# Optimization experiments

Measured on AMD Instinct MI355X. Metric: run time of the kernel, lower is better.

The kernel has to match this reference:

```python
import jax, jax.numpy as jnp
import numpy as np
from jax import lax

B, T, V, D, H = 32, 128, 32000, 512, 512


def setup_inputs() -> dict:
    key = jax.random.key(0)
    ks = jax.random.split(key, 8)
    s = 0.05  # keep gate pre-activations in a sane range
    return {
        "dst": jax.random.randint(ks[0], (B, T), 0, V),
        "E": jax.random.normal(ks[1], (V, D), jnp.float32) * s,
        "W_ih": jax.random.normal(ks[2], (4 * H, D + H), jnp.float32) * s,
        "W_hh": jax.random.normal(ks[3], (4 * H, H), jnp.float32) * s,
        "b_ih": jnp.zeros((4 * H,), jnp.float32),
        "b_hh": jnp.zeros((4 * H,), jnp.float32),
        "h0": jax.random.normal(ks[4], (B, H), jnp.float32) * s,
        "c0": jax.random.normal(ks[5], (B, H), jnp.float32) * s,
        "out0": jax.random.normal(ks[6], (B, H), jnp.float32) * s,
    }


def reference(dst, E, W_ih, W_hh, b_ih, b_hh, h0, c0, out0):
    # Embed targets: [B, T, D] -> time-major [T, B, D]
    emb_tbd = jnp.swapaxes(E[dst], 0, 1)

    def step(carry, e_t):
        h, c, out_prev = carry
        # input feeding: concat embedding with previous output -> [B, D+H]
        x = jnp.concatenate([e_t, out_prev], axis=1)
        gates = x @ W_ih.T + b_ih + h @ W_hh.T + b_hh  # [B, 4H]
        i, f, g, o = jnp.split(gates, 4, axis=1)
        i = jax.nn.sigmoid(i)
        f = jax.nn.sigmoid(f)
        g = jnp.tanh(g)
        o = jax.nn.sigmoid(o)
        c_new = f * c + i * g
        h_new = o * jnp.tanh(c_new)
        # attn is identity; dropout disabled (p=0 / eval)
        return (h_new, c_new, h_new), h_new

    _, outs_tbh = lax.scan(step, (h0, c0, out0), emb_tbd)  # [T, B, H]
    out_bth = jnp.swapaxes(outs_tbh, 0, 1)  # [B, T, H]
    # weight-tied projection to vocab + log softmax
    logits = jnp.einsum("bth,vh->btv", out_bth, E)  # [B, T, V]
    return jax.nn.log_softmax(logits, axis=-1)
```

## Files before the change

kernel.cpp:

```cpp
#include <hip/hip_runtime.h>
#include <hip/hip_bf16.h>
#include <math.h>

#define B_ 32
#define T_ 128
#define V_ 32000
#define D_ 512
#define H_ 512

typedef __attribute__((ext_vector_type(8))) short bf16x8;
typedef __attribute__((ext_vector_type(4))) float f32x4;
typedef __attribute__((ext_vector_type(2))) unsigned long long u64x2;

#define AS1 __attribute__((address_space(1)))
#define AS3 __attribute__((address_space(3)))

__device__ __forceinline__ unsigned short f2bf(float x) {
  unsigned int b = __float_as_uint(x);
  return (unsigned short)((b + 0x7FFFu + ((b >> 16) & 1u)) >> 16);
}
__device__ __forceinline__ float bf2f(unsigned short u) {
  return __uint_as_float(((unsigned int)u) << 16);
}
__device__ __forceinline__ float sigm(float x) { return 1.0f / (1.0f + __expf(-x)); }
__device__ __forceinline__ float tanh_fast(float x) { return 1.0f - 2.0f / (__expf(2.0f * x) + 1.0f); }

__device__ __forceinline__ unsigned long long ald64(const unsigned long long* p) {
  return __hip_atomic_load(p, __ATOMIC_RELAXED, __HIP_MEMORY_SCOPE_AGENT);
}
__device__ __forceinline__ unsigned ald32(const unsigned* p) {
  return __hip_atomic_load(p, __ATOMIC_RELAXED, __HIP_MEMORY_SCOPE_AGENT);
}

__global__ __launch_bounds__(64) void embed_bf_kernel(const int* __restrict__ dst,
                                                      const float* __restrict__ E,
                                                      unsigned short* __restrict__ embbf) {
  int rt = blockIdx.x;
  int t = rt >> 5, b = rt & 31;
  int v = dst[b * T_ + t];
  const float4* src = (const float4*)(E + (size_t)v * D_);
  ushort4* d = (ushort4*)(embbf + (size_t)rt * D_);
  #pragma unroll
  for (int r = 0; r < 2; ++r) {
    float4 x = src[threadIdx.x + r * 64];
    ushort4 o; o.x = f2bf(x.x); o.y = f2bf(x.y); o.z = f2bf(x.z); o.w = f2bf(x.w);
    d[threadIdx.x + r * 64] = o;
  }
}

__global__ void cvt_kernel(const float* __restrict__ in, unsigned short* __restrict__ out, int n4) {
  int stride = gridDim.x * blockDim.x;
  for (int i = blockIdx.x * blockDim.x + threadIdx.x; i < n4; i += stride) {
    float4 v = ((const float4*)in)[i];
    ushort4 o; o.x = f2bf(v.x); o.y = f2bf(v.y); o.z = f2bf(v.z); o.w = f2bf(v.w);
    ((ushort4*)out)[i] = o;
  }
}

__global__ void cvt_w1_kernel(const float* __restrict__ Wih, unsigned short* __restrict__ W1bf, int n4) {
  int stride = gridDim.x * blockDim.x;
  for (int i = blockIdx.x * blockDim.x + threadIdx.x; i < n4; i += stride) {
    int flat = i * 4;
    int r = flat >> 9, c = flat & 511;
    float4 v = *(const float4*)(Wih + (size_t)r * 1024 + c);
    ushort4 o; o.x = f2bf(v.x); o.y = f2bf(v.y); o.z = f2bf(v.z); o.w = f2bf(v.w);
    ((ushort4*)W1bf)[i] = o;
  }
}

__global__ void wr_prep_swz_kernel(const float* __restrict__ Wih, const float* __restrict__ Whh,
                                   unsigned short* __restrict__ Wrs, int n4) {
  int stride = gridDim.x * blockDim.x;
  for (int i = blockIdx.x * blockDim.x + threadIdx.x; i < n4; i += stride) {
    int flat = i * 4;
    int grow = flat >> 9, k = flat & 511;
    float4 a = *(const float4*)(Wih + (size_t)grow * 1024 + 512 + k);
    float4 b = ((const float4*)Whh)[i];
    ushort4 o;
    o.x = f2bf(a.x + b.x); o.y = f2bf(a.y + b.y); o.z = f2bf(a.z + b.z); o.w = f2bf(a.w + b.w);
    int gate = grow >> 9, kgl = grow & 511;
    int orow = (kgl >> 5) * 128 + (kgl & 31) * 4 + gate;
    int chunk = (k >> 3) ^ (orow & 7);
    *(ushort4*)(Wrs + (size_t)orow * 512 + chunk * 8 + (k & 7)) = o;
  }
}

__global__ __launch_bounds__(256) void gemm_pre_kernel(
    const unsigned short* __restrict__ A,
    const unsigned short* __restrict__ Bm,
    const float* __restrict__ bih, const float* __restrict__ bhh,
    unsigned short* __restrict__ preA3)
{
  __shared__ unsigned short ldsA[2][128 * 32];
  __shared__ unsigned short ldsB[2][128 * 32];
  const int tid = threadIdx.x;
  const int lane = tid & 63;
  const int wid = tid >> 6;
  const int wm = wid >> 1, wn = wid & 1;
  const int m0 = blockIdx.y * 128;
  const int n0 = blockIdx.x * 128;
  const int srow = lane >> 2;
  const int scol = (lane & 3) * 8;

  f32x4 acc[4][4] = {};
  const int NK = 512 / 32;

  auto stage = [&](int kk, int buf) {
    const int k0 = kk * 32;
    #pragma unroll
    for (int c = 0; c < 2; ++c) {
      const int r = wid * 32 + c * 16;
      const unsigned short* sa = A  + (size_t)(m0 + r + srow) * 512 + k0 + scol;
      const unsigned short* sb = Bm + (size_t)(n0 + r + srow) * 512 + k0 + scol;
      __builtin_amdgcn_global_load_lds((const AS1 void*)sa, (AS3 void*)&ldsA[buf][r * 32], 16, 0, 0);
      __builtin_amdgcn_global_load_lds((const AS1 void*)sb, (AS3 void*)&ldsB[buf][r * 32], 16, 0, 0);
    }
  };

  stage(0, 0);
  __syncthreads();

  const int rl = lane & 15;
  const int kb = lane >> 4;

  for (int kk = 0; kk < NK; ++kk) {
    const int buf = kk & 1;
    if (kk + 1 < NK) stage(kk + 1, buf ^ 1);
    const bf16x8* Af = (const bf16x8*)&ldsA[buf][0];
    const bf16x8* Bf = (const bf16x8*)&ldsB[buf][0];
    bf16x8 av[4], bv[4];
    #pragma unroll
    for (int mi = 0; mi < 4; ++mi) av[mi] = Af[(wm * 64 + mi * 16 + rl) * 4 + kb];
    #pragma unroll
    for (int ni = 0; ni < 4; ++ni) bv[ni] = Bf[(wn * 64 + ni * 16 + rl) * 4 + kb];
    #pragma unroll
    for (int mi = 0; mi < 4; ++mi)
      #pragma unroll
      for (int ni = 0; ni < 4; ++ni)
        acc[mi][ni] = __builtin_amdgcn_mfma_f32_16x16x32_bf16(av[mi], bv[ni], acc[mi][ni], 0, 0, 0);
    __syncthreads();
  }

  const int rb = (lane >> 4) * 4;
  #pragma unroll
  for (int mi = 0; mi < 4; ++mi)
    #pragma unroll
    for (int ni = 0; ni < 4; ++ni) {
      int mbase = m0 + wm * 64 + mi * 16 + rb;
      int col   = n0 + wn * 64 + ni * 16 + rl;
      int gate = col >> 9, kg = col & 511;
      int tt = mbase >> 5, bb0 = mbase & 31;
      float bb = bih[col] + bhh[col];
      #pragma unroll
      for (int j = 0; j < 4; ++j)
        preA3[(((size_t)tt * 512 + kg) * 32 + bb0 + j) * 4 + gate] = f2bf(acc[mi][ni][j] + bb);
    }
}

__global__ __launch_bounds__(256) void delta0_kernel(const float* __restrict__ Wih,
                                                     const float* __restrict__ out0,
                                                     const float* __restrict__ h0,
                                                     unsigned short* __restrict__ preA3) {
  const int r = blockIdx.x;
  const int tid = threadIdx.x;
  const int b = tid >> 3, seg = tid & 7;
  __shared__ float red[32][9];
  const float4* o4 = (const float4*)(out0 + (size_t)b * 512 + seg * 64);
  const float4* h4 = (const float4*)(h0 + (size_t)b * 512 + seg * 64);
  const float4* w4 = (const float4*)(Wih + (size_t)r * 1024 + 512 + seg * 64);
  float s = 0.f;
  #pragma unroll
  for (int j = 0; j < 16; ++j) {
    float4 o = o4[j], h = h4[j], w = w4[j];
    s += (o.x - h.x) * w.x + (o.y - h.y) * w.y + (o.z - h.z) * w.z + (o.w - h.w) * w.w;
  }
  red[b][seg] = s;
  __syncthreads();
  if (tid < 32) {
    float t = 0.f;
    #pragma unroll
    for (int j = 0; j < 8; ++j) t += red[tid][j];
    int gate = r >> 9, kgl = r & 511;
    unsigned short* p = preA3 + ((size_t)kgl * 32 + tid) * 4 + gate;
    *p = f2bf(bf2f(*p) + t);
  }
}

__global__ __launch_bounds__(1024) void mega_kernel(
    const unsigned short* __restrict__ Wrs,
    const unsigned short* __restrict__ preA3,
    const float* __restrict__ c0,
    unsigned short* __restrict__ hb0,
    unsigned short* __restrict__ hb1,
    unsigned short* __restrict__ Abf,
    unsigned int* __restrict__ flags,
    const unsigned short* __restrict__ Ebf,
    float* __restrict__ C,
    float* __restrict__ pmax, float* __restrict__ psum)
{
  __shared__ __align__(16) char smem[163840];
  const int tid = threadIdx.x, bid = blockIdx.x;
  const int lane = tid & 63, wid = tid >> 6;

  if (bid < 16) {
    unsigned short* wlds = (unsigned short*)smem;
    char* hx = smem + 131072;

    #pragma unroll
    for (int it = 0; it < 8; ++it) {
      int r = it * 16 + wid;
      const unsigned short* src = Wrs + ((size_t)bid * 128 + r) * 512 + lane * 8;
      __builtin_amdgcn_global_load_lds((const AS1 void*)src, (AS3 void*)&wlds[r * 512], 16, 0, 0);
    }

    const int myhalf = wid >> 3;
    const int rt = wid & 7;
    const int q = lane >> 4, rl = lane & 15;
    const int kg = bid * 32 + rt * 4 + q;
    const int b = myhalf * 16 + rl;
    float c_reg = c0[(size_t)b * 512 + kg];

    const int row = rt * 16 + rl;
    const char* wbase = (const char*)wlds + row * 1024;
    const int rx = (row & 7) << 4;
    const int hxs = (rl & 7) << 4;

    const int sw = wid & 7;
    const int sr = sw * 2 + (lane >> 5);
    const int sc = lane & 31;
    const int sblk = sc >> 1;
    const int srx = (sr & 7) << 4;
    const int sofs = sc * 32;

    if (myhalf == 0) {
      const unsigned long long* src =
          (const unsigned long long*)(hb0 + (size_t)sr * 512) + sc * 4;
      unsigned long long d0 = ald64(src + 0), d1 = ald64(src + 1);
      unsigned long long d2 = ald64(src + 2), d3 = ald64(src + 3);
      char* dst = hx + sr * 1024;
      u64x2 w0; w0[0] = d0; w0[1] = d1;
      u64x2 w1; w1[0] = d2; w1[1] = d3;
      *(u64x2*)(dst + (sofs ^ srx)) = w0;
      *(u64x2*)(dst + ((sofs + 16) ^ srx)) = w1;
    }
    __syncthreads();

    for (int p = 0; p < 2 * T_; ++p) {
      const int t = p >> 1, ph = p & 1, buf = p & 1;

      if (myhalf == ph) {
        unsigned long long pre =
            *(const unsigned long long*)(preA3 + (((size_t)t * 512 + kg) * 32 + b) * 4);
        const char* hbase = hx + buf * 16384 + rl * 1024;
        f32x4 acc = {}, acc2 = {};
        #pragma unroll
        for (int kk = 0; kk < 16; kk += 2) {
          int k0 = kk * 32 + q * 8;
          int k1 = k0 + 32;
          bf16x8 av0 = *(const bf16x8*)(wbase + ((k0 * 2) ^ rx));
          bf16x8 bv0 = *(const bf16x8*)(hbase + ((k0 * 2) ^ hxs));
          bf16x8 av1 = *(const bf16x8*)(wbase + ((k1 * 2) ^ rx));
          bf16x8 bv1 = *(const bf16x8*)(hbase + ((k1 * 2) ^ hxs));
          acc  = __builtin_amdgcn_mfma_f32_16x16x32_bf16(av0, bv0, acc, 0, 0, 0);
          acc2 = __builtin_amdgcn_mfma_f32_16x16x32_bf16(av1, bv1, acc2, 0, 0, 0);
        }
        float g0 = acc[0] + acc2[0] + bf2f((unsigned short)(pre));
        float g1 = acc[1] + acc2[1] + bf2f((unsigned short)(pre >> 16));
        float g2 = acc[2] + acc2[2] + bf2f((unsigned short)(pre >> 32));
        float g3 = acc[3] + acc2[3] + bf2f((unsigned short)(pre >> 48));
        float iv = sigm(g0), fv = sigm(g1), gv = tanh_fast(g2), ov = sigm(g3);
        float cn = fv * c_reg + iv * gv;
        c_reg = cn;
        float hn = ov * tanh_fast(cn);
        int hv = (int)f2bf(hn);
        int nb = __shfl(hv, lane + 16);
        if ((q & 1) == 0) {
          unsigned pair = (unsigned)hv | ((unsigned)nb << 16);
          if (t != T_ - 1) {
            unsigned short* hout = ((t + 1) & 1) ? hb1 : hb0;
            __hip_atomic_store((unsigned int*)(hout + (size_t)b * 512 + kg), pair,
                               __ATOMIC_RELAXED, __HIP_MEMORY_SCOPE_AGENT);
          }
          __hip_atomic_store((unsigned int*)(Abf + ((size_t)t * 32 + b) * 512 + kg), pair,
                             __ATOMIC_RELAXED, __HIP_MEMORY_SCOPE_AGENT);
        }
      } else if (p + 1 < 2 * T_) {
        const int t2 = (p + 1) >> 1;
        if (t2 > 0) {
          const unsigned* fl = &flags[(myhalf * 16 + sblk) * 16];
          unsigned spins = 0;
          while (ald32(fl) < (unsigned)t2) {
            if (++spins > 1000000u) break;
          }
        }
        const unsigned short* hsrc = (t2 & 1) ? hb1 : hb0;
        const unsigned long long* src =
            (const unsigned long long*)(hsrc + (size_t)(myhalf * 16 + sr) * 512) + sc * 4;
        unsigned long long d0 = ald64(src + 0), d1 = ald64(src + 1);
        unsigned long long d2 = ald64(src + 2), d3 = ald64(src + 3);
        char* dst = hx + (buf ^ 1) * 16384 + sr * 1024;
        u64x2 w0; w0[0] = d0; w0[1] = d1;
        u64x2 w1; w1[0] = d2; w1[1] = d3;
        *(u64x2*)(dst + (sofs ^ srx)) = w0;
        *(u64x2*)(dst + ((sofs + 16) ^ srx)) = w1;
      }

      __syncthreads();

      if (tid == ph * 512)
        __hip_atomic_store(&flags[(ph * 16 + bid) * 16], (unsigned)(t + 1),
                           __ATOMIC_RELAXED, __HIP_MEMORY_SCOPE_AGENT);
    }
    return;
  }

  const int e = bid - 16;
  const int n_t = e % 250, m_t = e / 250;
  const int m0 = m_t * 256, n0 = n_t * 128;

  if (tid == 0) {
    unsigned spins = 0;
    if (m_t == 15) {
      for (int i = 0; i < 32; ++i)
        while (ald32(&flags[i * 16]) < 128u) {
          __builtin_amdgcn_s_sleep(8);
          if (++spins > 3000000u) break;
        }
    } else {
      const unsigned want1 = (unsigned)(8 * m_t + 9);
      while (ald32(&flags[0]) < want1 || ald32(&flags[256]) < want1) {
        __builtin_amdgcn_s_sleep(8);
        if (++spins > 3000000u) break;
      }
    }
  }
  __syncthreads();

  unsigned short* Al[2] = { (unsigned short*)smem, (unsigned short*)(smem + 16384) };
  unsigned short* Bb[2] = { (unsigned short*)(smem + 32768), (unsigned short*)(smem + 40960) };
  float (*smax)[256] = (float (*)[256])(smem + 49152);
  float (*ssum)[256] = (float (*)[256])(smem + 53248);

  const int trow = tid >> 2, tcol = tid & 3;
  const int wm = wid >> 2, wn = wid & 3;
  const int rl = lane & 15, kb = lane >> 4;

  auto stageP = [&](int kk, int bf) {
    {
      u64x2 w = *(const u64x2*)(Abf + (size_t)(m0 + trow) * 512 + kk * 32 + tcol * 8);
      *(u64x2*)((char*)Al[bf] + trow * 64 + ((tcol ^ ((trow >> 1) & 3)) * 16)) = w;
    }
    if (tid < 512) {
      int br = tid >> 2, bc = tid & 3;
      u64x2 w = *(const u64x2*)(Ebf + (size_t)(n0 + br) * 512 + kk * 32 + bc * 8);
      *(u64x2*)((char*)Bb[bf] + br * 64 + ((bc ^ ((br >> 1) & 3)) * 16)) = w;
    }
  };

  f32x4 acc[4][2] = {};
  stageP(0, 0);
  __syncthreads();

  for (int kk = 0; kk < 16; ++kk) {
    const int bf = kk & 1;
    if (kk + 1 < 16) stageP(kk + 1, bf ^ 1);
    bf16x8 bv[2];
    #pragma unroll
    for (int y = 0; y < 2; ++y) {
      int br = wn * 32 + y * 16 + rl;
      bv[y] = *(const bf16x8*)((char*)Bb[bf] + br * 64 + ((kb ^ ((br >> 1) & 3)) * 16));
    }
    #pragma unroll
    for (int x = 0; x < 4; ++x) {
      int ar = wm * 64 + x * 16 + rl;
      bf16x8 av = *(const bf16x8*)((char*)Al[bf] + ar * 64 + ((kb ^ ((ar >> 1) & 3)) * 16));
      #pragma unroll
      for (int y = 0; y < 2; ++y)
        acc[x][y] = __builtin_amdgcn_mfma_f32_16x16x32_bf16(av, bv[y], acc[x][y], 0, 0, 0);
    }
    __syncthreads();
  }

  #pragma unroll
  for (int x = 0; x < 4; ++x)
    #pragma unroll
    for (int y = 0; y < 2; ++y) {
      int col = n0 + wn * 32 + y * 16 + rl;
      #pragma unroll
      for (int j = 0; j < 4; ++j) {
        int arow = m0 + wm * 64 + x * 16 + kb * 4 + j;
        size_t crow = (size_t)(arow & 31) * T_ + (arow >> 5);
        __builtin_nontemporal_store(acc[x][y][j], &C[crow * (size_t)V_ + col]);
      }
    }

  #pragma unroll
  for (int x = 0; x < 4; ++x)
    #pragma unroll
    for (int j = 0; j < 4; ++j) {
      float m = fmaxf(acc[x][0][j], acc[x][1][j]);
      m = fmaxf(m, __shfl_xor(m, 1)); m = fmaxf(m, __shfl_xor(m, 2));
      m = fmaxf(m, __shfl_xor(m, 4)); m = fmaxf(m, __shfl_xor(m, 8));
      if (rl == 0) smax[wn][wm * 64 + x * 16 + kb * 4 + j] = m;
    }
  __syncthreads();
  #pragma unroll
  for (int x = 0; x < 4; ++x)
    #pragma unroll
    for (int j = 0; j < 4; ++j) {
      int rowl = wm * 64 + x * 16 + kb * 4 + j;
      float M = fmaxf(fmaxf(smax[0][rowl], smax[1][rowl]),
                      fmaxf(smax[2][rowl], smax[3][rowl]));
      float s = __expf(acc[x][0][j] - M) + __expf(acc[x][1][j] - M);
      s += __shfl_xor(s, 1); s += __shfl_xor(s, 2);
      s += __shfl_xor(s, 4); s += __shfl_xor(s, 8);
      if (rl == 0) ssum[wn][rowl] = s;
    }
  __syncthreads();
  if (tid < 256) {
    float M = fmaxf(fmaxf(smax[0][tid], smax[1][tid]),
                    fmaxf(smax[2][tid], smax[3][tid]));
    float S = ssum[0][tid] + ssum[1][tid] + ssum[2][tid] + ssum[3][tid];
    pmax[(size_t)(m0 + tid) * 256 + n_t] = M;
    psum[(size_t)(m0 + tid) * 256 + n_t] = S;
  }
}

__global__ __launch_bounds__(256) void softmax_finish_kernel(
    float* __restrict__ C, const float* __restrict__ pmax, const float* __restrict__ psum) {
  const size_t row = blockIdx.x;
  const int b = blockIdx.x >> 7, t = blockIdx.x & 127;
  const size_t arow = (size_t)t * 32 + b;
  const int tid = threadIdx.x, lane = tid & 63, wid = tid >> 6;
  __shared__ float red[4];

  float pm = (tid < 250) ? pmax[arow * 256 + tid] : -INFINITY;
  float ps = (tid < 250) ? psum[arow * 256 + tid] : 0.f;

  float m = pm;
  #pragma unroll
  for (int off = 32; off > 0; off >>= 1) m = fmaxf(m, __shfl_xor(m, off));
  if (lane == 0) red[wid] = m;
  __syncthreads();
  m = fmaxf(fmaxf(red[0], red[1]), fmaxf(red[2], red[3]));
  __syncthreads();

  float s = (tid < 250) ? ps * __expf(pm - m) : 0.f;
  #pragma unroll
  for (int off = 32; off > 0; off >>= 1) s += __shfl_xor(s, off);
  if (lane == 0) red[wid] = s;
  __syncthreads();
  s = red[0] + red[1] + red[2] + red[3];
  const float lse = m + logf(s);

  f32x4* p4 = (f32x4*)(C + row * (size_t)V_);
  for (int i = tid; i < 8000; i += 256) {
    f32x4 v = p4[i];
    v -= lse;
    __builtin_nontemporal_store(v, &p4[i]);
  }
}

extern "C" void kernel_launch(void* const* d_in, const int* in_sizes, int n_in,
                              void* d_out, int out_size, void* d_ws, size_t ws_size,
                              hipStream_t stream) {
  const int*   dst  = (const int*)d_in[0];
  const float* E    = (const float*)d_in[1];
  const float* Wih  = (const float*)d_in[2];
  const float* Whh  = (const float*)d_in[3];
  const float* bih  = (const float*)d_in[4];
  const float* bhh  = (const float*)d_in[5];
  const float* h0   = (const float*)d_in[6];
  const float* c0   = (const float*)d_in[7];
  const float* out0 = (const float*)d_in[8];
  float* C = (float*)d_out;

  char* ws = (char*)d_ws;
  unsigned short* Ebf   = (unsigned short*)(ws);
  unsigned short* preA3 = (unsigned short*)(ws + (size_t)33554432);
  unsigned short* Wrs   = (unsigned short*)(ws + (size_t)50331648);
  unsigned short* embbf = (unsigned short*)(ws + (size_t)52428800);
  float*          pmax  = (float*)(ws + (size_t)52428800);
  unsigned short* W1bf  = (unsigned short*)(ws + (size_t)56623104);
  float*          psum  = (float*)(ws + (size_t)56623104);
  unsigned short* Abf   = (unsigned short*)(ws + (size_t)60817408);
  unsigned short* hb0   = (unsigned short*)(ws + (size_t)65011712);
  unsigned short* hb1   = (unsigned short*)(ws + (size_t)65044480);
  unsigned int*   flg   = (unsigned int*)(ws + (size_t)65077248);

  (void)hipMemsetAsync(flg, 0, 2048, stream);

  embed_bf_kernel<<<dim3(T_ * B_), dim3(64), 0, stream>>>(dst, E, embbf);
  cvt_kernel<<<dim3(2048), dim3(256), 0, stream>>>(E, Ebf, V_ * D_ / 4);
  cvt_w1_kernel<<<dim3(256), dim3(256), 0, stream>>>(Wih, W1bf, 2048 * 512 / 4);
  wr_prep_swz_kernel<<<dim3(256), dim3(256), 0, stream>>>(Wih, Whh, Wrs, 2048 * 512 / 4);

  gemm_pre_kernel<<<dim3(2048 / 128, 4096 / 128), dim3(256), 0, stream>>>(embbf, W1bf, bih, bhh, preA3);
  delta0_kernel<<<dim3(2048), dim3(256), 0, stream>>>(Wih, out0, h0, preA3);
  cvt_kernel<<<dim3(16), dim3(256), 0, stream>>>(h0, hb0, B_ * H_ / 4);

  mega_kernel<<<dim3(16 + 16 * 250), dim3(1024), 0, stream>>>(
      Wrs, preA3, c0, hb0, hb1, Abf, flg, Ebf, C, pmax, psum);

  softmax_finish_kernel<<<dim3(B_ * T_), dim3(256), 0, stream>>>(C, pmax, psum);
}
```

Measured before the change: 976.8 us.

## Fold softmax finish into mega kernel via per-row-tile completion counters

Removes the separate softmax_finish launch and appends 64 finisher blocks per 256-row tile to the mega kernel. Each finisher spins on a per-tile done counter that the GEMM blocks increment, then normalises 4 rows with 1024 threads. The aim is to overlap the log-softmax normalisation of early row tiles with the recurrence and the projection of later tiles. In exchange, C stores become relaxed atomic stores instead of nontemporal stores, and there is a spin-wait deadlock risk if finisher blocks occupy CUs before their producers are scheduled.

```diff
diff --git a/kernel.cpp b/kernel.cpp
--- a/kernel.cpp
+++ b/kernel.cpp
@@ -30,6 +30,12 @@
 }
 __device__ __forceinline__ unsigned ald32(const unsigned* p) {
   return __hip_atomic_load(p, __ATOMIC_RELAXED, __HIP_MEMORY_SCOPE_AGENT);
+}
+__device__ __forceinline__ float aldf(const float* p) {
+  return __uint_as_float(__hip_atomic_load((const unsigned*)p, __ATOMIC_RELAXED, __HIP_MEMORY_SCOPE_AGENT));
+}
+__device__ __forceinline__ void astf(float* p, float v) {
+  __hip_atomic_store((unsigned*)p, __float_as_uint(v), __ATOMIC_RELAXED, __HIP_MEMORY_SCOPE_AGENT);
 }
 
 __global__ __launch_bounds__(64) void embed_bf_kernel(const int* __restrict__ dst,
@@ -201,6 +207,7 @@
   __shared__ __align__(16) char smem[163840];
   const int tid = threadIdx.x, bid = blockIdx.x;
   const int lane = tid & 63, wid = tid >> 6;
+  unsigned int* done = flags + 512;
 
   if (bid < 16) {
     unsigned short* wlds = (unsigned short*)smem;
@@ -315,146 +322,164 @@
   }
 
   const int e = bid - 16;
-  const int n_t = e % 250, m_t = e / 250;
-  const int m0 = m_t * 256, n0 = n_t * 128;
-
-  if (tid == 0) {
-    unsigned spins = 0;
-    if (m_t == 15) {
-      for (int i = 0; i < 32; ++i)
-        while (ald32(&flags[i * 16]) < 128u) {
+  const int m_t = e / 314, rr = e % 314;
+  const int m0 = m_t * 256;
+
+  if (rr < 250) {
+    const int n_t = rr;
+    const int n0 = n_t * 128;
+
+    if (tid == 0) {
+      unsigned spins = 0;
+      if (m_t == 15) {
+        for (int i = 0; i < 32; ++i)
+          while (ald32(&flags[i * 16]) < 128u) {
+            __builtin_amdgcn_s_sleep(8);
+            if (++spins > 3000000u) break;
+          }
+      } else {
+        const unsigned want1 = (unsigned)(8 * m_t + 9);
+        while (ald32(&flags[0]) < want1 || ald32(&flags[256]) < want1) {
           __builtin_amdgcn_s_sleep(8);
           if (++spins > 3000000u) break;
         }
-    } else {
-      const unsigned want1 = (unsigned)(8 * m_t + 9);
-      while (ald32(&flags[0]) < want1 || ald32(&flags[256]) < want1) {
-        __builtin_amdgcn_s_sleep(8);
-        if (++spins > 3000000u) break;
-      }
+      }
+    }
+    __syncthreads();
+
+    unsigned short* Al[2] = { (unsigned short*)smem, (unsigned short*)(smem + 16384) };
+    unsigned short* Bb[2] = { (unsigned short*)(smem + 32768), (unsigned short*)(smem + 40960) };
+    float (*smax)[256] = (float (*)[256])(smem + 49152);
+    float (*ssum)[256] = (float (*)[256])(smem + 53248);
+
+    const int trow = tid >> 2, tcol = tid & 3;
+    const int wm = wid >> 2, wn = wid & 3;
+    const int rl = lane & 15, kb = lane >> 4;
+
+    auto stageP = [&](int kk, int bf) {
+      {
+        u64x2 w = *(const u64x2*)(Abf + (size_t)(m0 + trow) * 512 + kk * 32 + tcol * 8);
+        *(u64x2*)((char*)Al[bf] + trow * 64 + ((tcol ^ ((trow >> 1) & 3)) * 16)) = w;
+      }
+      if (tid < 512) {
+        int br = tid >> 2, bc = tid & 3;
+        u64x2 w = *(const u64x2*)(Ebf + (size_t)(n0 + br) * 512 + kk * 32 + bc * 8);
+        *(u64x2*)((char*)Bb[bf] + br * 64 + ((bc ^ ((br >> 1) & 3)) * 16)) = w;
+      }
+    };
+
+    f32x4 acc[4][2] = {};
+    stageP(0, 0);
+    __syncthreads();
+
+    for (int kk = 0; kk < 16; ++kk) {
+      const int bf = kk & 1;
+      if (kk + 1 < 16) stageP(kk + 1, bf ^ 1);
+      bf16x8 bv[2];
+      #pragma unroll
+      for (int y = 0; y < 2; ++y) {
+        int br = wn * 32 + y * 16 + rl;
+        bv[y] = *(const bf16x8*)((char*)Bb[bf] + br * 64 + ((kb ^ ((br >> 1) & 3)) * 16));
+      }
+      #pragma unroll
+      for (int x = 0; x < 4; ++x) {
+        int ar = wm * 64 + x * 16 + rl;
+        bf16x8 av = *(const bf16x8*)((char*)Al[bf] + ar * 64 + ((kb ^ ((ar >> 1) & 3)) * 16));
+        #pragma unroll
+        for (int y = 0; y < 2; ++y)
+          acc[x][y] = __builtin_amdgcn_mfma_f32_16x16x32_bf16(av, bv[y], acc[x][y], 0, 0, 0);
+      }
+      __syncthreads();
+    }
+
+    #pragma unroll
+    for (int x = 0; x < 4; ++x)
+      #pragma unroll
+      for (int y = 0; y < 2; ++y) {
+        int col = n0 + wn * 32 + y * 16 + rl;
+        #pragma unroll
+        for (int j = 0; j < 4; ++j) {
+          int arow = m0 + wm * 64 + x * 16 + kb * 4 + j;
+          size_t crow = (size_t)(arow & 31) * T_ + (arow >> 5);
+          astf(&C[crow * (size_t)V_ + col], acc[x][y][j]);
+        }
+      }
+
+    #pragma unroll
+    for (int x = 0; x < 4; ++x)
+      #pragma unroll
+      for (int j = 0; j < 4; ++j) {
+        float m = fmaxf(acc[x][0][j], acc[x][1][j]);
+        m = fmaxf(m, __shfl_xor(m, 1)); m = fmaxf(m, __shfl_xor(m, 2));
+        m = fmaxf(m, __shfl_xor(m, 4)); m = fmaxf(m, __shfl_xor(m, 8));
+        if (rl == 0) smax[wn][wm * 64 + x * 16 + kb * 4 + j] = m;
+      }
+    __syncthreads();
+    #pragma unroll
+    for (int x = 0; x < 4; ++x)
+      #pragma unroll
+      for (int j = 0; j < 4; ++j) {
+        int rowl = wm * 64 + x * 16 + kb * 4 + j;
+        float M = fmaxf(fmaxf(smax[0][rowl], smax[1][rowl]),
+                        fmaxf(smax[2][rowl], smax[3][rowl]));
+        float s = __expf(acc[x][0][j] - M) + __expf(acc[x][1][j] - M);
+        s += __shfl_xor(s, 1); s += __shfl_xor(s, 2);
+        s += __shfl_xor(s, 4); s += __shfl_xor(s, 8);
+        if (rl == 0) ssum[wn][rowl] = s;
+      }
+    __syncthreads();
+    if (tid < 256) {
+      float M = fmaxf(fmaxf(smax[0][tid], smax[1][tid]),
+                      fmaxf(smax[2][tid], smax[3][tid]));
+      float S = ssum[0][tid] + ssum[1][tid] + ssum[2][tid] + ssum[3][tid];
+      __hip_atomic_store(&pmax[(size_t)(m0 + tid) * 256 + n_t], M,
+                         __ATOMIC_RELAXED, __HIP_MEMORY_SCOPE_AGENT);
+      __hip_atomic_store(&psum[(size_t)(m0 + tid) * 256 + n_t], S,
+                         __ATOMIC_RELAXED, __HIP_MEMORY_SCOPE_AGENT);
+    }
+    __syncthreads();
+    if (tid == 0)
+      __hip_atomic_fetch_add(&done[m_t * 16], 1u, __ATOMIC_RELAXED, __HIP_MEMORY_SCOPE_AGENT);
+    return;
+  }
+
+  const int fb = rr - 250;
+  if (tid == 0) {
+    unsigned spins = 0;
+    while (ald32(&done[m_t * 16]) < 250u) {
+      __builtin_amdgcn_s_sleep(16);
+      if (++spins > 3000000u) break;
     }
   }
   __syncthreads();
 
-  unsigned short* Al[2] = { (unsigned short*)smem, (unsigned short*)(smem + 16384) };
-  unsigned short* Bb[2] = { (unsigned short*)(smem + 32768), (unsigned short*)(smem + 40960) };
-  float (*smax)[256] = (float (*)[256])(smem + 49152);
-  float (*ssum)[256] = (float (*)[256])(smem + 53248);
-
-  const int trow = tid >> 2, tcol = tid & 3;
-  const int wm = wid >> 2, wn = wid & 3;
-  const int rl = lane & 15, kb = lane >> 4;
-
-  auto stageP = [&](int kk, int bf) {
-    {
-      u64x2 w = *(const u64x2*)(Abf + (size_t)(m0 + trow) * 512 + kk * 32 + tcol * 8);
-      *(u64x2*)((char*)Al[bf] + trow * 64 + ((tcol ^ ((trow >> 1) & 3)) * 16)) = w;
-    }
-    if (tid < 512) {
-      int br = tid >> 2, bc = tid & 3;
-      u64x2 w = *(const u64x2*)(Ebf + (size_t)(n0 + br) * 512 + kk * 32 + bc * 8);
-      *(u64x2*)((char*)Bb[bf] + br * 64 + ((bc ^ ((br >> 1) & 3)) * 16)) = w;
-    }
-  };
-
-  f32x4 acc[4][2] = {};
-  stageP(0, 0);
-  __syncthreads();
-
-  for (int kk = 0; kk < 16; ++kk) {
-    const int bf = kk & 1;
-    if (kk + 1 < 16) stageP(kk + 1, bf ^ 1);
-    bf16x8 bv[2];
-    #pragma unroll
-    for (int y = 0; y < 2; ++y) {
-      int br = wn * 32 + y * 16 + rl;
-      bv[y] = *(const bf16x8*)((char*)Bb[bf] + br * 64 + ((kb ^ ((br >> 1) & 3)) * 16));
-    }
-    #pragma unroll
-    for (int x = 0; x < 4; ++x) {
-      int ar = wm * 64 + x * 16 + rl;
-      bf16x8 av = *(const bf16x8*)((char*)Al[bf] + ar * 64 + ((kb ^ ((ar >> 1) & 3)) * 16));
-      #pragma unroll
-      for (int y = 0; y < 2; ++y)
-        acc[x][y] = __builtin_amdgcn_mfma_f32_16x16x32_bf16(av, bv[y], acc[x][y], 0, 0, 0);
-    }
-    __syncthreads();
-  }
-
-  #pragma unroll
-  for (int x = 0; x < 4; ++x)
-    #pragma unroll
-    for (int y = 0; y < 2; ++y) {
-      int col = n0 + wn * 32 + y * 16 + rl;
-      #pragma unroll
-      for (int j = 0; j < 4; ++j) {
-        int arow = m0 + wm * 64 + x * 16 + kb * 4 + j;
-        size_t crow = (size_t)(arow & 31) * T_ + (arow >> 5);
-        __builtin_nontemporal_store(acc[x][y][j], &C[crow * (size_t)V_ + col]);
-      }
-    }
-
-  #pragma unroll
-  for (int x = 0; x < 4; ++x)
-    #pragma unroll
-    for (int j = 0; j < 4; ++j) {
-      float m = fmaxf(acc[x][0][j], acc[x][1][j]);
-      m = fmaxf(m, __shfl_xor(m, 1)); m = fmaxf(m, __shfl_xor(m, 2));
-      m = fmaxf(m, __shfl_xor(m, 4)); m = fmaxf(m, __shfl_xor(m, 8));
-      if (rl == 0) smax[wn][wm * 64 + x * 16 + kb * 4 + j] = m;
-    }
-  __syncthreads();
-  #pragma unroll
-  for (int x = 0; x < 4; ++x)
-    #pragma unroll
-    for (int j = 0; j < 4; ++j) {
-      int rowl = wm * 64 + x * 16 + kb * 4 + j;
-      float M = fmaxf(fmaxf(smax[0][rowl], smax[1][rowl]),
-                      fmaxf(smax[2][rowl], smax[3][rowl]));
-      float s = __expf(acc[x][0][j] - M) + __expf(acc[x][1][j] - M);
-      s += __shfl_xor(s, 1); s += __shfl_xor(s, 2);
-      s += __shfl_xor(s, 4); s += __shfl_xor(s, 8);
-      if (rl == 0) ssum[wn][rowl] = s;
-    }
-  __syncthreads();
-  if (tid < 256) {
-    float M = fmaxf(fmaxf(smax[0][tid], smax[1][tid]),
-                    fmaxf(smax[2][tid], smax[3][tid]));
-    float S = ssum[0][tid] + ssum[1][tid] + ssum[2][tid] + ssum[3][tid];
-    pmax[(size_t)(m0 + tid) * 256 + n_t] = M;
-    psum[(size_t)(m0 + tid) * 256 + n_t] = S;
-  }
-}
-
-__global__ __launch_bounds__(256) void softmax_finish_kernel(
-    float* __restrict__ C, const float* __restrict__ pmax, const float* __restrict__ psum) {
-  const size_t row = blockIdx.x;
-  const int b = blockIdx.x >> 7, t = blockIdx.x & 127;
-  const size_t arow = (size_t)t * 32 + b;
-  const int tid = threadIdx.x, lane = tid & 63, wid = tid >> 6;
-  __shared__ float red[4];
-
-  float pm = (tid < 250) ? pmax[arow * 256 + tid] : -INFINITY;
-  float ps = (tid < 250) ? psum[arow * 256 + tid] : 0.f;
+  float (*red)[4] = (float (*)[4])smem;
+  const int g = tid >> 8, lt = tid & 255;
+  const int wig = (tid >> 6) & 3;
+  const int arow = m0 + fb * 4 + g;
+
+  float pm = (lt < 250) ? aldf(&pmax[(size_t)arow * 256 + lt]) : -INFINITY;
+  float ps = (lt < 250) ? aldf(&psum[(size_t)arow * 256 + lt]) : 0.f;
 
   float m = pm;
   #pragma unroll
   for (int off = 32; off > 0; off >>= 1) m = fmaxf(m, __shfl_xor(m, off));
-  if (lane == 0) red[wid] = m;
+  if (lane == 0) red[g][wig] = m;
   __syncthreads();
-  m = fmaxf(fmaxf(red[0], red[1]), fmaxf(red[2], red[3]));
+  m = fmaxf(fmaxf(red[g][0], red[g][1]), fmaxf(red[g][2], red[g][3]));
   __syncthreads();
 
-  float s = (tid < 250) ? ps * __expf(pm - m) : 0.f;
+  float s = (lt < 250) ? ps * __expf(pm - m) : 0.f;
   #pragma unroll
   for (int off = 32; off > 0; off >>= 1) s += __shfl_xor(s, off);
-  if (lane == 0) red[wid] = s;
+  if (lane == 0) red[g][wig] = s;
   __syncthreads();
-  s = red[0] + red[1] + red[2] + red[3];
+  s = red[g][0] + red[g][1] + red[g][2] + red[g][3];
   const float lse = m + logf(s);
 
-  f32x4* p4 = (f32x4*)(C + row * (size_t)V_);
-  for (int i = tid; i < 8000; i += 256) {
+  const size_t crow = (size_t)(arow & 31) * T_ + (arow >> 5);
+  f32x4* p4 = (f32x4*)(C + crow * (size_t)V_);
+  for (int i = lt; i < 8000; i += 256) {
     f32x4 v = p4[i];
     v -= lse;
     __builtin_nontemporal_store(v, &p4[i]);
@@ -488,7 +513,7 @@
   unsigned short* hb1   = (unsigned short*)(ws + (size_t)65044480);
   unsigned int*   flg   = (unsigned int*)(ws + (size_t)65077248);
 
-  (void)hipMemsetAsync(flg, 0, 2048, stream);
+  (void)hipMemsetAsync(flg, 0, 4096, stream);
 
   embed_bf_kernel<<<dim3(T_ * B_), dim3(64), 0, stream>>>(dst, E, embbf);
   cvt_kernel<<<dim3(2048), dim3(256), 0, stream>>>(E, Ebf, V_ * D_ / 4);
@@ -499,8 +524,6 @@
   delta0_kernel<<<dim3(2048), dim3(256), 0, stream>>>(Wih, out0, h0, preA3);
   cvt_kernel<<<dim3(16), dim3(256), 0, stream>>>(h0, hb0, B_ * H_ / 4);
 
-  mega_kernel<<<dim3(16 + 16 * 250), dim3(1024), 0, stream>>>(
+  mega_kernel<<<dim3(16 + 16 * 314), dim3(1024), 0, stream>>>(
       Wrs, preA3, c0, hb0, hb1, Abf, flg, Ebf, C, pmax, psum);
-
-  softmax_finish_kernel<<<dim3(B_ * T_), dim3(256), 0, stream>>>(C, pmax, psum);
-}
+}
```

Measured after the change: 968.8 us. About the same (-0.8%).
